# Performance work log

Measured on AMD Instinct MI355X. Metric: run time of the kernel, lower is better.

The kernel has to match this reference:

```python
import jax, jax.numpy as jnp
import numpy as np

B, S, DIM = 2, 2048, 2048
NH, NKV = 16, 4
HD = DIM // NH
BASE, FACTOR = 10000.0, 1.0
WINDOW, STRIDE = 256, 64


def setup_inputs() -> dict:
    key = jax.random.key(0)
    ks = jax.random.split(key, 5)
    x = jax.random.normal(ks[0], (B, S, DIM), jnp.float32)
    Wq = jax.random.normal(ks[1], (DIM, DIM), jnp.float32) * 0.02
    Wkv = jax.random.normal(ks[2], (2 * NKV * HD, DIM), jnp.float32) * 0.02
    Wo = jax.random.normal(ks[3], (DIM, DIM), jnp.float32) * 0.02
    Wr = jax.random.normal(ks[4], (NH, DIM), jnp.float32) * 0.02
    br = jnp.zeros((NH,), jnp.float32)
    return {"x": x, "Wq": Wq, "Wkv": Wkv, "Wo": Wo, "Wr": Wr, "br": br}


def _rope_cos_sin(seqlen, start_pos):
    half = HD // 2
    inv_freq = 1.0 / (BASE ** (jnp.arange(0, half, dtype=jnp.float32) * 2.0 / HD))
    inv_freq = inv_freq / FACTOR  # YaRN position interpolation; FACTOR=1 -> vanilla RoPE
    mscale = float(0.1 * np.log(FACTOR) + 1.0) if FACTOR > 1.0 else 1.0
    t = jnp.arange(start_pos, start_pos + seqlen, dtype=jnp.float32)
    freqs = t[:, None] * inv_freq[None, :]  # [S, HD/2]
    return jnp.cos(freqs) * mscale, jnp.sin(freqs) * mscale


def _apply_rope(x, cos, sin):
    # x: [B, H, S, HD]; rotate-half convention
    x1, x2 = jnp.split(x, 2, axis=-1)
    return jnp.concatenate([x1 * cos - x2 * sin, x2 * cos + x1 * sin], axis=-1)


def reference(x, Wq, Wkv, Wo, Wr, br):
    scale = 1.0 / np.sqrt(HD)
    # projections
    q = (x @ Wq.T).reshape(B, S, NH, HD).transpose(0, 2, 1, 3)        # [B,NH,S,HD]
    kv = (x @ Wkv.T).reshape(B, S, 2, NKV, HD)
    k = kv[:, :, 0].transpose(0, 2, 1, 3)                              # [B,NKV,S,HD]
    v = kv[:, :, 1].transpose(0, 2, 1, 3)
    # RoPE (start_pos = 0)
    cos, sin = _rope_cos_sin(S, 0)
    cos, sin = cos[None, None], sin[None, None]
    q = _apply_rope(q, cos, sin)
    k = _apply_rope(k, cos, sin)
    # GQA expansion (repeat_interleave over head axis)
    rep = NH // NKV
    k = jnp.repeat(k, rep, axis=1)                                     # [B,NH,S,HD]
    v = jnp.repeat(v, rep, axis=1)
    # per-head sigmoid routing gate on q
    head_w = jax.nn.sigmoid(x @ Wr.T + br)                             # [B,S,NH]
    q = q * head_w.transpose(0, 2, 1)[..., None]
    # local windowed causal attention
    qi = jnp.arange(S)[:, None]
    ki = jnp.arange(S)[None, :]
    mask = (ki <= qi) & (ki >= qi - WINDOW)                            # [S,S]
    scores = jnp.einsum('bhqd,bhkd->bhqk', q, k) * scale
    scores = jnp.where(mask, scores, -1e30)
    attn_local = jnp.einsum('bhqk,bhkd->bhqd', jax.nn.softmax(scores, axis=-1), v)
    # strided global attention (non-causal over subsampled keys)
    g_idx = jnp.arange(0, S, STRIDE)
    kg, vg = k[:, :, g_idx], v[:, :, g_idx]                            # [B,NH,S/STRIDE,HD]
    gscores = jnp.einsum('bhqd,bhkd->bhqk', q, kg) * scale
    attn_global = jnp.einsum('bhqk,bhkd->bhqd', jax.nn.softmax(gscores, axis=-1), vg)
    out = 0.7 * attn_local + 0.3 * attn_global
    out = out.transpose(0, 2, 1, 3).reshape(B, S, DIM)
    return out @ Wo.T
```

## Files before the change

kernel.cpp:

```cpp
#include <hip/hip_runtime.h>
#include <stdint.h>

typedef unsigned short u16;
typedef uint32_t u32;
typedef __bf16 bf16x8 __attribute__((ext_vector_type(8)));
typedef u16    u16x8  __attribute__((ext_vector_type(8)));
typedef float  f32x4  __attribute__((ext_vector_type(4)));
typedef u32    u32x4v __attribute__((ext_vector_type(4)));

constexpr int Bc = 2, Sc = 2048, DIMc = 2048, NHc = 16, NKVc = 4, HDc = 128;
constexpr int Mc  = Bc * Sc;
constexpr int QKVN = 3072;
constexpr float SCALE = 0.08838834764831845f;

__device__ __forceinline__ u16 f2bf(float f) {
    uint32_t u = __builtin_bit_cast(uint32_t, f);
    u += 0x7FFFu + ((u >> 16) & 1u);
    return (u16)(u >> 16);
}
__device__ __forceinline__ u32 pk2bf(float a, float b) {
    return (u32)f2bf(a) | ((u32)f2bf(b) << 16);
}

__device__ __forceinline__ void async_cp16(const u16* gsrc, u16* ldst) {
    __builtin_amdgcn_global_load_lds(
        (__attribute__((address_space(1))) void*)(gsrc),
        (__attribute__((address_space(3))) void*)(ldst), 16, 0, 0);
}

constexpr int HWB = Mc;
constexpr int CQ1 = DIMc * DIMc / 4;
constexpr int CQ2 = 1024 * DIMc / 4;
constexpr int CQ3 = DIMc * DIMc / 4;
constexpr int NWQ = (CQ1 + CQ2 + CQ3) / 256;
constexpr int NTB = Sc * 64 / 256;
__global__ __launch_bounds__(256) void cvt_hw(const float* __restrict__ x,
                                              const float* __restrict__ Wq,
                                              const float* __restrict__ Wkv,
                                              const float* __restrict__ Wo,
                                              const float* __restrict__ Wr,
                                              const float* __restrict__ br,
                                              u16* __restrict__ xb,
                                              u16* __restrict__ Wqkvb,
                                              u16* __restrict__ Wob,
                                              float* __restrict__ hw,
                                              float2* __restrict__ csT) {
    __shared__ __align__(16) float xs[2048];
    int bid = blockIdx.x;
    if (bid < HWB) {
        const int m = bid;
        const float4* xg = (const float4*)(x + (size_t)m * 2048);
        float4* xs4 = (float4*)xs;
        for (int i = threadIdx.x; i < 512; i += 256) xs4[i] = xg[i];
        __syncthreads();
        {
            ushort4* dst = (ushort4*)(xb + (size_t)m * 2048);
            for (int i = threadIdx.x; i < 512; i += 256) {
                float4 v = xs4[i];
                ushort4 o;
                o.x = f2bf(v.x); o.y = f2bf(v.y); o.z = f2bf(v.z); o.w = f2bf(v.w);
                dst[i] = o;
            }
        }
        const int wid = threadIdx.x >> 6, lane = threadIdx.x & 63;
#pragma unroll 1
        for (int h = wid; h < NHc; h += 4) {
            const float4* wr4 = (const float4*)(Wr + (size_t)h * 2048);
            float s = 0.f;
#pragma unroll
            for (int j = 0; j < 8; j++) {
                float4 xv = xs4[lane + j * 64];
                float4 wv = wr4[lane + j * 64];
                s += xv.x * wv.x + xv.y * wv.y + xv.z * wv.z + xv.w * wv.w;
            }
#pragma unroll
            for (int off = 32; off; off >>= 1) s += __shfl_xor(s, off, 64);
            if (lane == 0) hw[m * NHc + h] = 1.f / (1.f + __expf(-(s + br[h])));
        }
        return;
    }
    bid -= HWB;
    if (bid < NWQ) {
        int q = bid * 256 + threadIdx.x;
        const float* src; u16* dst; int qi;
        if (q < CQ1)                 { src = Wq;  dst = Wqkvb; qi = q; }
        else if ((q -= CQ1) < CQ2)   { src = Wkv; dst = Wqkvb + (size_t)DIMc * DIMc; qi = q; }
        else                         { q -= CQ2;  src = Wo;  dst = Wob; qi = q; }
        float4 v = ((const float4*)src)[qi];
        ushort4 o;
        o.x = f2bf(v.x); o.y = f2bf(v.y); o.z = f2bf(v.z); o.w = f2bf(v.w);
        ((ushort4*)dst)[qi] = o;
        return;
    }
    bid -= NWQ;
    int idx = bid * 256 + threadIdx.x;
    int s = idx >> 6, d = idx & 63;
    float invf = powf(10000.0f, -(float)d * (1.0f / 64.0f));
    float ang = (float)s * invf;
    float2 cs;
    cs.x = cosf(ang);
    cs.y = sinf(ang);
    csT[idx] = cs;
}

__global__ __launch_bounds__(512, 2) void gemm_qkv(const u16* __restrict__ A,
                                                   const u16* __restrict__ Bw,
                                                   const float* __restrict__ hw,
                                                   const float2* __restrict__ csT,
                                                   u16* __restrict__ Qr,
                                                   u16* __restrict__ Kb,
                                                   u16* __restrict__ Vt,
                                                   u16* __restrict__ Vg) {
    __shared__ __align__(16) u16 SM[4][2][128 * 64];
    float* EpS = (float*)SM;
    const int Kd = DIMc;
    constexpr int NT = 32;
    const int tid  = threadIdx.x;
    const int lane = tid & 63;
    const int wid  = tid >> 6;
    const int m0 = blockIdx.y * 256;
    const int n0 = blockIdx.x * 256;
    const int wr = wid >> 2;
    const int wc = wid & 3;
    const int fr = lane & 15;
    const int fq = lane >> 4;
    const int f7 = fr & 7;

    const int s0 = tid, s1 = tid + 512;
    const int r0 = s0 >> 3, r1 = s1 >> 3;
    const int j0 = (s0 & 7) ^ (r0 & 7), j1 = (s1 & 7) ^ (r1 & 7);
    const u16* gA0 = A  + (size_t)(m0 + r0) * Kd + j0 * 8;
    const u16* gA1 = A  + (size_t)(m0 + r1) * Kd + j1 * 8;
    const u16* gB0 = Bw + (size_t)(n0 + r0) * Kd + j0 * 8;
    const u16* gB1 = Bw + (size_t)(n0 + r1) * Kd + j1 * 8;
    const size_t hK = (size_t)128 * Kd;

    auto stA = [&](int buf, int h, int t) {
        async_cp16(gA0 + h * hK + t * 64, &SM[buf][h][s0 * 8]);
        async_cp16(gA1 + h * hK + t * 64, &SM[buf][h][s1 * 8]);
    };
    auto stB = [&](int buf, int h, int t) {
        async_cp16(gB0 + h * hK + t * 64, &SM[2 + buf][h][s0 * 8]);
        async_cp16(gB1 + h * hK + t * 64, &SM[2 + buf][h][s1 * 8]);
    };

    f32x4 acc[8][4];
#pragma unroll
    for (int i = 0; i < 8; i++)
#pragma unroll
        for (int j = 0; j < 4; j++) {
            f32x4 z = {0.f, 0.f, 0.f, 0.f};
            acc[i][j] = z;
        }

    const int c0 = ((fq) ^ f7) * 8;
    const int c1 = ((4 + fq) ^ f7) * 8;
    bf16x8 afl[4][2], afh[4][2], bfl[2][2], bfh[2][2];

    auto rdA = [&](bf16x8 (&af)[4][2], int tb, int mh) {
        const u16* Ab = SM[tb][wr];
#pragma unroll
        for (int m2 = 0; m2 < 4; m2++) {
            int row = (mh * 4 + m2) * 16 + fr;
            af[m2][0] = __builtin_bit_cast(bf16x8, *(const u16x8*)(Ab + row * 64 + c0));
            af[m2][1] = __builtin_bit_cast(bf16x8, *(const u16x8*)(Ab + row * 64 + c1));
        }
    };
    auto rdB = [&](bf16x8 (&bf)[2][2], int tb, int nh) {
        const u16* Bb = SM[2 + tb][wc >> 1];
#pragma unroll
        for (int n2 = 0; n2 < 2; n2++) {
            int row = (wc & 1) * 64 + (nh * 2 + n2) * 16 + fr;
            bf[n2][0] = __builtin_bit_cast(bf16x8, *(const u16x8*)(Bb + row * 64 + c0));
            bf[n2][1] = __builtin_bit_cast(bf16x8, *(const u16x8*)(Bb + row * 64 + c1));
        }
    };
    auto mma = [&](bf16x8 (&af)[4][2], bf16x8 (&bf)[2][2], int mh, int nh) {
        __builtin_amdgcn_s_setprio(1);
#pragma unroll
        for (int m2 = 0; m2 < 4; m2++)
#pragma unroll
            for (int n2 = 0; n2 < 2; n2++) {
                acc[mh * 4 + m2][nh * 2 + n2] =
                    __builtin_amdgcn_mfma_f32_16x16x32_bf16(af[m2][0], bf[n2][0],
                                                            acc[mh * 4 + m2][nh * 2 + n2], 0, 0, 0);
                acc[mh * 4 + m2][nh * 2 + n2] =
                    __builtin_amdgcn_mfma_f32_16x16x32_bf16(af[m2][1], bf[n2][1],
                                                            acc[mh * 4 + m2][nh * 2 + n2], 0, 0, 0);
            }
        __builtin_amdgcn_s_setprio(0);
    };

#define LGK0 do { asm volatile("s_waitcnt lgkmcnt(0)" ::: "memory"); \
                  __builtin_amdgcn_sched_barrier(0); } while (0)
#define BAR  __builtin_amdgcn_s_barrier()

    stA(0, 0, 0); stA(0, 1, 0); stB(0, 0, 0); stB(0, 1, 0);
    stB(1, 0, 1); stB(1, 1, 1);
    asm volatile("s_waitcnt vmcnt(4)" ::: "memory");
    BAR;

#pragma unroll 1
    for (int i = 0; i < NT / 2; i++) {
        const int t0 = 2 * i, t1 = 2 * i + 1;
        rdA(afl, 0, 0); rdB(bfl, 0, 0);
        stA(1, 0, t1);
        BAR; LGK0; mma(afl, bfl, 0, 0); BAR;
        rdB(bfh, 0, 1);
        stA(1, 1, t1);
        BAR; LGK0; mma(afl, bfh, 0, 1); BAR;
        rdA(afh, 0, 1);
        if (t0 + 2 < NT) stB(0, 0, t0 + 2);
        BAR; LGK0; mma(afh, bfl, 1, 0); BAR;
        if (t0 + 2 < NT) {
            stB(0, 1, t0 + 2);
            asm volatile("s_waitcnt vmcnt(4)" ::: "memory");
        } else {
            asm volatile("s_waitcnt vmcnt(0)" ::: "memory");
        }
        BAR; __builtin_amdgcn_sched_barrier(0); mma(afh, bfh, 1, 1); BAR;
        rdA(afl, 1, 0); rdB(bfl, 1, 0);
        if (t0 + 2 < NT) stA(0, 0, t0 + 2);
        BAR; LGK0; mma(afl, bfl, 0, 0); BAR;
        rdB(bfh, 1, 1);
        if (t0 + 2 < NT) stA(0, 1, t0 + 2);
        BAR; LGK0; mma(afl, bfh, 0, 1); BAR;
        rdA(afh, 1, 1);
        if (t1 + 2 < NT) stB(1, 0, t1 + 2);
        BAR; LGK0; mma(afh, bfl, 1, 0); BAR;
        if (t1 + 2 < NT) {
            stB(1, 1, t1 + 2);
            asm volatile("s_waitcnt vmcnt(4)" ::: "memory");
        } else {
            asm volatile("s_waitcnt vmcnt(0)" ::: "memory");
        }
        BAR; __builtin_amdgcn_sched_barrier(0); mma(afh, bfh, 1, 1); BAR;
    }
#undef LGK0
#undef BAR

    const int tL = n0 >> 7;
    const int bb = m0 >> 11;
    const int sb_t = m0 & 2047;
#pragma unroll
    for (int p = 0; p < 4; p++) {
        __syncthreads();
        if (wr == (p >> 1)) {
#pragma unroll
            for (int m2 = 0; m2 < 4; m2++) {
#pragma unroll
                for (int nj = 0; nj < 4; nj++) {
                    int lr = m2 * 16 + fq * 4;
                    int col = wc * 64 + nj * 16 + fr;
#pragma unroll
                    for (int r = 0; r < 4; r++)
                        EpS[(lr + r) * 261 + col] = acc[(p & 1) * 4 + m2][nj][r];
                }
            }
        }
        __syncthreads();
        const int sbase = sb_t + p * 64;
        if (tL < 20) {
            const int d = tid & 63, rg = tid >> 6;
#pragma unroll 1
            for (int ch = 0; ch < 2; ch++) {
                const int t = tL + ch;
#pragma unroll
                for (int tt = 0; tt < 8; tt++) {
                    int lr = rg + 8 * tt;
                    int s = sbase + lr;
                    float v1 = EpS[lr * 261 + ch * 128 + d];
                    float v2 = EpS[lr * 261 + ch * 128 + 64 + d];
                    float2 cs = csT[(s << 6) + d];
                    float o1 = v1 * cs.x - v2 * cs.y;
                    float o2 = v2 * cs.x + v1 * cs.y;
                    if (t < 16) {
                        float w = hw[(size_t)((bb << 11) + s) * NHc + t] * SCALE;
                        size_t g = ((size_t)(bb * NHc + t) << 11) + s;
                        Qr[g * HDc + d]      = f2bf(o1 * w);
                        Qr[g * HDc + 64 + d] = f2bf(o2 * w);
                    } else {
                        size_t g = ((size_t)(bb * NKVc + (t - 16)) << 11) + s;
                        Kb[g * HDc + d]      = f2bf(o1);
                        Kb[g * HDc + 64 + d] = f2bf(o2);
                    }
                }
            }
        } else {
            const int sl = tid & 63, dg = tid >> 6;
            const int sg = sbase + sl;
#pragma unroll 1
            for (int ch = 0; ch < 2; ch++) {
                const int bhv = bb * NKVc + (tL + ch - 20);
                u16* Vbase = Vt + (size_t)bhv * HDc * Sc;
#pragma unroll
                for (int tt = 0; tt < 16; tt++) {
                    int d = dg + 8 * tt;
                    u16 bv = f2bf(EpS[sl * 261 + ch * 128 + d]);
                    Vbase[(size_t)d * Sc + sg] = bv;
                    if ((sg & 63) == 0)
                        Vg[(size_t)bhv * 4096 + d * 32 + (sg >> 6)] = bv;
                }
            }
        }
    }
}

__global__ __launch_bounds__(512, 2) void gemm_bt3(const u16* __restrict__ A,
                                                   const u16* __restrict__ Bw,
                                                   float* __restrict__ C,
                                                   int Mdim, int Ndim, int Kdim) {
    __shared__ __align__(16) u16 As[2][256 * 64];
    __shared__ __align__(16) u16 Bs[2][128 * 64];
    const int tid  = threadIdx.x;
    const int lane = tid & 63;
    const int wid  = tid >> 6;
    const int m0 = blockIdx.y * 256;
    const int n0 = blockIdx.x * 128;
    const int wm = (wid >> 1) * 64;
    const int wn = (wid & 1) * 64;
    const int fr = lane & 15;
    const int fq = lane >> 4;
    const int f7 = fr & 7;

    const u16* gA[4]; const u16* gB[2];
    int sOffA[4], sOffB[2];
#pragma unroll
    for (int q = 0; q < 4; q++) {
        int s = tid + q * 512;
        int row = s >> 3;
        int j = (s & 7) ^ (row & 7);
        gA[q] = A + (size_t)(m0 + row) * Kdim + j * 8;
        sOffA[q] = s * 8;
    }
#pragma unroll
    for (int q = 0; q < 2; q++) {
        int s = tid + q * 512;
        int row = s >> 3;
        int j = (s & 7) ^ (row & 7);
        gB[q] = Bw + (size_t)(n0 + row) * Kdim + j * 8;
        sOffB[q] = s * 8;
    }

    f32x4 acc[4][4];
#pragma unroll
    for (int i = 0; i < 4; i++)
#pragma unroll
        for (int j = 0; j < 4; j++) {
            f32x4 z = {0.f, 0.f, 0.f, 0.f};
            acc[i][j] = z;
        }

    const int NT = Kdim >> 6;
    const int c0 = ((fq) ^ f7) * 8;
    const int c1 = ((4 + fq) ^ f7) * 8;

#pragma unroll
    for (int q = 0; q < 4; q++) async_cp16(gA[q], &As[0][sOffA[q]]);
#pragma unroll
    for (int q = 0; q < 2; q++) async_cp16(gB[q], &Bs[0][sOffB[q]]);
#pragma unroll
    for (int q = 0; q < 4; q++) async_cp16(gA[q] + 64, &As[1][sOffA[q]]);
#pragma unroll
    for (int q = 0; q < 2; q++) async_cp16(gB[q] + 64, &Bs[1][sOffB[q]]);

    for (int t = 0; t < NT; t++) {
        const u16* At = As[t & 1];
        const u16* Bt = Bs[t & 1];

        if (t + 1 < NT) {
            asm volatile("s_waitcnt vmcnt(6)" ::: "memory");
        } else {
            asm volatile("s_waitcnt vmcnt(0)" ::: "memory");
        }
        __builtin_amdgcn_s_barrier();

        bf16x8 af0[4], bf0[4];
#pragma unroll
        for (int i = 0; i < 4; i++)
            af0[i] = __builtin_bit_cast(bf16x8, *(const u16x8*)(At + (wm + i * 16 + fr) * 64 + c0));
#pragma unroll
        for (int j = 0; j < 4; j++)
            bf0[j] = __builtin_bit_cast(bf16x8, *(const u16x8*)(Bt + (wn + j * 16 + fr) * 64 + c0));
        asm volatile("s_waitcnt lgkmcnt(0)" ::: "memory");
        __builtin_amdgcn_sched_barrier(0);
        __builtin_amdgcn_s_setprio(1);
#pragma unroll
        for (int i = 0; i < 2; i++)
#pragma unroll
            for (int j = 0; j < 4; j++)
                acc[i][j] = __builtin_amdgcn_mfma_f32_16x16x32_bf16(af0[i], bf0[j], acc[i][j], 0, 0, 0);
        __builtin_amdgcn_s_setprio(0);

        bf16x8 af1[4], bf1[4];
#pragma unroll
        for (int i = 0; i < 4; i++)
            af1[i] = __builtin_bit_cast(bf16x8, *(const u16x8*)(At + (wm + i * 16 + fr) * 64 + c1));
#pragma unroll
        for (int j = 0; j < 4; j++)
            bf1[j] = __builtin_bit_cast(bf16x8, *(const u16x8*)(Bt + (wn + j * 16 + fr) * 64 + c1));
        __builtin_amdgcn_s_setprio(1);
#pragma unroll
        for (int i = 2; i < 4; i++)
#pragma unroll
            for (int j = 0; j < 4; j++)
                acc[i][j] = __builtin_amdgcn_mfma_f32_16x16x32_bf16(af0[i], bf0[j], acc[i][j], 0, 0, 0);
        __builtin_amdgcn_s_setprio(0);
        asm volatile("s_waitcnt lgkmcnt(0)" ::: "memory");
        __builtin_amdgcn_sched_barrier(0);
        __builtin_amdgcn_s_barrier();

        if (t + 2 < NT) {
#pragma unroll
            for (int q = 0; q < 4; q++)
                async_cp16(gA[q] + (size_t)(t + 2) * 64, &As[t & 1][sOffA[q]]);
        }
        __builtin_amdgcn_s_setprio(1);
#pragma unroll
        for (int i = 0; i < 2; i++)
#pragma unroll
            for (int j = 0; j < 4; j++)
                acc[i][j] = __builtin_amdgcn_mfma_f32_16x16x32_bf16(af1[i], bf1[j], acc[i][j], 0, 0, 0);
        __builtin_amdgcn_s_setprio(0);

        if (t + 2 < NT) {
#pragma unroll
            for (int q = 0; q < 2; q++)
                async_cp16(gB[q] + (size_t)(t + 2) * 64, &Bs[t & 1][sOffB[q]]);
        }
        __builtin_amdgcn_s_setprio(1);
#pragma unroll
        for (int i = 2; i < 4; i++)
#pragma unroll
            for (int j = 0; j < 4; j++)
                acc[i][j] = __builtin_amdgcn_mfma_f32_16x16x32_bf16(af1[i], bf1[j], acc[i][j], 0, 0, 0);
        __builtin_amdgcn_s_setprio(0);
    }

#pragma unroll
    for (int i = 0; i < 4; i++)
#pragma unroll
        for (int j = 0; j < 4; j++) {
            int row = m0 + wm + i * 16 + fq * 4;
            int col = n0 + wn + j * 16 + fr;
#pragma unroll
            for (int r = 0; r < 4; r++)
                C[(size_t)(row + r) * Ndim + col] = acc[i][j][r];
        }
}

__device__ __forceinline__ float colreduce_max(f32x4 a, f32x4 b) {
    float m = fmaxf(fmaxf(fmaxf(a[0], a[1]), fmaxf(a[2], a[3])),
                    fmaxf(fmaxf(b[0], b[1]), fmaxf(b[2], b[3])));
    m = fmaxf(m, __shfl_xor(m, 16, 64));
    m = fmaxf(m, __shfl_xor(m, 32, 64));
    return m;
}

__device__ __forceinline__ bf16x8 build_pfrag(u32 pk0, u32 pk1, u32 pk2, u32 pk3, int lane) {
    const int c = lane & 15, Q = lane >> 4;
    const int sl0 = ((Q & 1) * 2) * 16 + c;
    const int sl1 = sl0 + 16;
    u32 a0 = (u32)__shfl((int)pk0, sl0, 64), b0 = (u32)__shfl((int)pk2, sl0, 64);
    u32 a1 = (u32)__shfl((int)pk1, sl0, 64), b1 = (u32)__shfl((int)pk3, sl0, 64);
    u32 a2 = (u32)__shfl((int)pk0, sl1, 64), b2 = (u32)__shfl((int)pk2, sl1, 64);
    u32 a3 = (u32)__shfl((int)pk1, sl1, 64), b3 = (u32)__shfl((int)pk3, sl1, 64);
    const bool hi = Q >= 2;
    u32x4v r = { hi ? b0 : a0, hi ? b1 : a1, hi ? b2 : a2, hi ? b3 : a3 };
    return __builtin_bit_cast(bf16x8, r);
}

__global__ __launch_bounds__(256) void attn3(const u16* __restrict__ Qr,
                                             const u16* __restrict__ Kb,
                                             const u16* __restrict__ Vt,
                                             const u16* __restrict__ Vg,
                                             u16* __restrict__ attnb) {
    __shared__ __align__(16) u16 Ksh[2 * 4096];
    __shared__ __align__(16) u16 Vsh[2 * 4096];
    const int tid  = threadIdx.x;
    const int lane = tid & 63, wid = tid >> 6;
    const int bid  = blockIdx.x;
    const int q64  = (31 - (bid >> 5)) << 6;
    const int bh   = bid & 31;
    const int h    = bh & 15;
    const int b    = bh >> 4;
    const int qw   = q64 + wid * 16;
    const int c = lane & 15, Q = lane >> 4;
    const int kvh = h >> 2;

    const u16* Qp = Qr + ((size_t)((b * NHc + h) * Sc + qw)) * HDc;
    const u16* Kh = Kb + (size_t)(b * NKVc + kvh) * Sc * HDc;
    const u16* Vh = Vt + (size_t)(b * NKVc + kvh) * HDc * Sc;
    const u16* Vgh = Vg + (size_t)(b * NKVc + kvh) * HDc * 32;

    const int kp0 = (q64 >= 256) ? (q64 - 256) : 0;
    const int nstages = (q64 + 64 - kp0) >> 5;

    auto stageLoad = [&](int bufi, int kp) {
        u16* Kd = Ksh + bufi * 4096;
        u16* Vd = Vsh + bufi * 4096;
#pragma unroll
        for (int qq = 0; qq < 2; qq++) {
            int s = tid + qq * 256;
            int kr = s >> 4;
            int jk = (s & 15) ^ (kr & 15);
            async_cp16(Kh + (size_t)(kp + kr) * HDc + jk * 8, Kd + s * 8);
            int dv = s >> 2;
            int jv = (s & 3) ^ ((dv >> 2) & 3);
            async_cp16(Vh + (size_t)dv * Sc + kp + jv * 8, Vd + s * 8);
        }
    };

    bf16x8 qf[4];
#pragma unroll
    for (int ch = 0; ch < 4; ch++)
        qf[ch] = __builtin_bit_cast(bf16x8, *(const u16x8*)(Qp + c * HDc + ch * 32 + Q * 8));

    stageLoad(0, kp0);

    f32x4 sg0 = {0.f,0.f,0.f,0.f}, sg1 = {0.f,0.f,0.f,0.f};
#pragma unroll
    for (int ch = 0; ch < 4; ch++) {
        bf16x8 k0 = __builtin_bit_cast(bf16x8, *(const u16x8*)(Kh + ((size_t)c << 6) * HDc + ch * 32 + Q * 8));
        bf16x8 k1 = __builtin_bit_cast(bf16x8, *(const u16x8*)(Kh + ((size_t)(c + 16) << 6) * HDc + ch * 32 + Q * 8));
        sg0 = __builtin_amdgcn_mfma_f32_16x16x32_bf16(k0, qf[ch], sg0, 0, 0, 0);
        sg1 = __builtin_amdgcn_mfma_f32_16x16x32_bf16(k1, qf[ch], sg1, 0, 0, 0);
    }
    float mg = colreduce_max(sg0, sg1);
    f32x4 pg0, pg1;
    float gsum = 0.f;
#pragma unroll
    for (int r = 0; r < 4; r++) {
        pg0[r] = __expf(sg0[r] - mg);
        pg1[r] = __expf(sg1[r] - mg);
        gsum += pg0[r] + pg1[r];
    }
    gsum += __shfl_xor(gsum, 16, 64);
    gsum += __shfl_xor(gsum, 32, 64);
    const float lG = gsum;
    bf16x8 pgf = build_pfrag(pk2bf(pg0[0], pg0[1]), pk2bf(pg0[2], pg0[3]),
                             pk2bf(pg1[0], pg1[1]), pk2bf(pg1[2], pg1[3]), lane);
    f32x4 OG[8];
#pragma unroll
    for (int dt = 0; dt < 8; dt++) {
        bf16x8 vf = __builtin_bit_cast(bf16x8, *(const u16x8*)(Vgh + (dt * 16 + c) * 32 + Q * 8));
        f32x4 z = {0.f, 0.f, 0.f, 0.f};
        OG[dt] = __builtin_amdgcn_mfma_f32_16x16x32_bf16(vf, pgf, z, 0, 0, 0);
    }

    f32x4 OL[8];
#pragma unroll
    for (int dt = 0; dt < 8; dt++) { f32x4 z = {0.f,0.f,0.f,0.f}; OL[dt] = z; }
    float mL = -1e30f, lL = 0.f;

    for (int ip = 0; ip < nstages; ip++) {
        const int kp = kp0 + ip * 32;
        __syncthreads();
        if (ip + 1 < nstages) stageLoad((ip + 1) & 1, kp + 32);
        const u16* Kd = Ksh + (ip & 1) * 4096;
        const u16* Vd = Vsh + (ip & 1) * 4096;

        if (kp > qw + 15 || kp + 31 < qw - 256) continue;

        f32x4 s0 = {0.f,0.f,0.f,0.f}, s1 = {0.f,0.f,0.f,0.f};
#pragma unroll
        for (int ch = 0; ch < 4; ch++) {
            int jj = ch * 4 + Q;
            bf16x8 k0 = __builtin_bit_cast(bf16x8, *(const u16x8*)(Kd + (c * 16 + (jj ^ c)) * 8));
            bf16x8 k1 = __builtin_bit_cast(bf16x8, *(const u16x8*)(Kd + ((16 + c) * 16 + (jj ^ c)) * 8));
            s0 = __builtin_amdgcn_mfma_f32_16x16x32_bf16(k0, qf[ch], s0, 0, 0, 0);
            s1 = __builtin_amdgcn_mfma_f32_16x16x32_bf16(k1, qf[ch], s1, 0, 0, 0);
        }
        if ((kp + 31 > qw) || (kp < qw - 241)) {
            const int q = qw + c;
#pragma unroll
            for (int r = 0; r < 4; r++) {
                int kk0 = kp + Q * 4 + r;
                int kk1 = kk0 + 16;
                if (kk0 > q || kk0 + 256 < q) s0[r] = -1e30f;
                if (kk1 > q || kk1 + 256 < q) s1[r] = -1e30f;
            }
        }
        float mx = colreduce_max(s0, s1);
        float mnew = fmaxf(mL, mx);
        float alpha = __expf(mL - mnew);
        f32x4 p0, p1;
        float sum = 0.f;
#pragma unroll
        for (int r = 0; r < 4; r++) {
            p0[r] = __expf(s0[r] - mnew);
            p1[r] = __expf(s1[r] - mnew);
            sum += p0[r] + p1[r];
        }
        sum += __shfl_xor(sum, 16, 64);
        sum += __shfl_xor(sum, 32, 64);
        lL = lL * alpha + sum;
        mL = mnew;
        bf16x8 pf = build_pfrag(pk2bf(p0[0], p0[1]), pk2bf(p0[2], p0[3]),
                                pk2bf(p1[0], p1[1]), pk2bf(p1[2], p1[3]), lane);
#pragma unroll
        for (int dt = 0; dt < 8; dt++) {
            int d = dt * 16 + c;
            bf16x8 vf = __builtin_bit_cast(bf16x8, *(const u16x8*)(Vd + (d * 4 + (Q ^ (c >> 2))) * 8));
            OL[dt] = OL[dt] * alpha;
            OL[dt] = __builtin_amdgcn_mfma_f32_16x16x32_bf16(vf, pf, OL[dt], 0, 0, 0);
        }
    }

    const float rL = 0.7f / lL, rG = 0.3f / lG;
    u16* orow = attnb + ((size_t)(b * Sc + qw + c)) * DIMc + h * HDc;
#pragma unroll
    for (int dt = 0; dt < 8; dt++) {
        ushort4 ov;
        ov.x = f2bf(OL[dt][0] * rL + OG[dt][0] * rG);
        ov.y = f2bf(OL[dt][1] * rL + OG[dt][1] * rG);
        ov.z = f2bf(OL[dt][2] * rL + OG[dt][2] * rG);
        ov.w = f2bf(OL[dt][3] * rL + OG[dt][3] * rG);
        *(ushort4*)(orow + dt * 16 + Q * 4) = ov;
    }
}

extern "C" void kernel_launch(void* const* d_in, const int* in_sizes, int n_in,
                              void* d_out, int out_size, void* d_ws, size_t ws_size,
                              hipStream_t stream) {
    const float* x   = (const float*)d_in[0];
    const float* Wq  = (const float*)d_in[1];
    const float* Wkv = (const float*)d_in[2];
    const float* Wo  = (const float*)d_in[3];
    const float* Wr  = (const float*)d_in[4];
    const float* br  = (const float*)d_in[5];
    float* out = (float*)d_out;

    char* p = (char*)d_ws;
    u16* xb    = (u16*)p;   p += (size_t)Mc * DIMc * 2;
    u16* Wqkvb = (u16*)p;   p += (size_t)QKVN * DIMc * 2;
    u16* Wob   = (u16*)p;   p += (size_t)DIMc * DIMc * 2;
    float* hw  = (float*)p; p += (size_t)Mc * NHc * 4;
    float2* csT = (float2*)p; p += (size_t)Sc * 64 * 8;
    u16* Qrb   = (u16*)p;   p += (size_t)Mc * DIMc * 2;
    u16* Kb16  = (u16*)p;   p += (size_t)Bc * NKVc * Sc * HDc * 2;
    u16* Vt16  = (u16*)p;   p += (size_t)Bc * NKVc * HDc * Sc * 2;
    u16* Vg16  = (u16*)p;   p += (size_t)Bc * NKVc * HDc * 32 * 2;
    u16* attnb = (u16*)p;   p += (size_t)Mc * DIMc * 2;

    cvt_hw<<<HWB + NWQ + NTB, 256, 0, stream>>>(x, Wq, Wkv, Wo, Wr, br, xb, Wqkvb, Wob, hw, csT);

    dim3 gqkv(QKVN / 256, Mc / 256);
    gemm_qkv<<<gqkv, 512, 0, stream>>>(xb, Wqkvb, hw, csT, Qrb, Kb16, Vt16, Vg16);

    attn3<<<Bc * NHc * (Sc / 64), 256, 0, stream>>>(Qrb, Kb16, Vt16, Vg16, attnb);

    dim3 go(DIMc / 128, Mc / 256);
    gemm_bt3<<<go, 512, 0, stream>>>(attnb, Wob, out, Mc, DIMc, DIMc);
}
```

Baseline: 286.8 us.

## Restructure GEMM main loop into per-tile double-buffered pipeline with fewer barriers

Replaces the two-tile unrolled loop, which put a barrier pair around each of its eight MFMA quarter-blocks, with a single-tile loop. Each iteration issues all four LDS fragment reads up front, waits on partial lgkmcnt counts so MFMAs start as fragments arrive, and refills the freed buffer half with global loads for tile t+2. The intent is to cut barrier and LDS-wait stalls and overlap LDS reads with MFMA. In exchange it holds more fragments in flight, relies on exact vmcnt/lgkmcnt accounting, and prefetches both A and B for tile 1 in the prologue.

```diff
diff --git a/kernel.cpp b/kernel.cpp
--- a/kernel.cpp
+++ b/kernel.cpp
@@ -191,52 +191,43 @@
         __builtin_amdgcn_s_setprio(0);
     };
 
-#define LGK0 do { asm volatile("s_waitcnt lgkmcnt(0)" ::: "memory"); \
-                  __builtin_amdgcn_sched_barrier(0); } while (0)
+#define SB   __builtin_amdgcn_sched_barrier(0)
 #define BAR  __builtin_amdgcn_s_barrier()
 
     stA(0, 0, 0); stA(0, 1, 0); stB(0, 0, 0); stB(0, 1, 0);
-    stB(1, 0, 1); stB(1, 1, 1);
-    asm volatile("s_waitcnt vmcnt(4)" ::: "memory");
-    BAR;
+    stA(1, 0, 1); stA(1, 1, 1); stB(1, 0, 1); stB(1, 1, 1);
 
 #pragma unroll 1
-    for (int i = 0; i < NT / 2; i++) {
-        const int t0 = 2 * i, t1 = 2 * i + 1;
-        rdA(afl, 0, 0); rdB(bfl, 0, 0);
-        stA(1, 0, t1);
-        BAR; LGK0; mma(afl, bfl, 0, 0); BAR;
-        rdB(bfh, 0, 1);
-        stA(1, 1, t1);
-        BAR; LGK0; mma(afl, bfh, 0, 1); BAR;
-        rdA(afh, 0, 1);
-        if (t0 + 2 < NT) stB(0, 0, t0 + 2);
-        BAR; LGK0; mma(afh, bfl, 1, 0); BAR;
-        if (t0 + 2 < NT) {
-            stB(0, 1, t0 + 2);
-            asm volatile("s_waitcnt vmcnt(4)" ::: "memory");
+    for (int t = 0; t < NT; t++) {
+        const int b = t & 1;
+        if (t + 1 < NT) {
+            asm volatile("s_waitcnt vmcnt(8)" ::: "memory");
         } else {
             asm volatile("s_waitcnt vmcnt(0)" ::: "memory");
         }
-        BAR; __builtin_amdgcn_sched_barrier(0); mma(afh, bfh, 1, 1); BAR;
-        rdA(afl, 1, 0); rdB(bfl, 1, 0);
-        if (t0 + 2 < NT) stA(0, 0, t0 + 2);
-        BAR; LGK0; mma(afl, bfl, 0, 0); BAR;
-        rdB(bfh, 1, 1);
-        if (t0 + 2 < NT) stA(0, 1, t0 + 2);
-        BAR; LGK0; mma(afl, bfh, 0, 1); BAR;
-        rdA(afh, 1, 1);
-        if (t1 + 2 < NT) stB(1, 0, t1 + 2);
-        BAR; LGK0; mma(afh, bfl, 1, 0); BAR;
-        if (t1 + 2 < NT) {
-            stB(1, 1, t1 + 2);
-            asm volatile("s_waitcnt vmcnt(4)" ::: "memory");
-        } else {
-            asm volatile("s_waitcnt vmcnt(0)" ::: "memory");
-        }
-        BAR; __builtin_amdgcn_sched_barrier(0); mma(afh, bfh, 1, 1); BAR;
-    }
-#undef LGK0
+        BAR; SB;
+
+        rdA(afl, b, 0);
+        rdB(bfl, b, 0);
+        rdB(bfh, b, 1);
+        rdA(afh, b, 1);
+
+        asm volatile("s_waitcnt lgkmcnt(12)" ::: "memory"); SB;
+        mma(afl, bfl, 0, 0);
+        asm volatile("s_waitcnt lgkmcnt(8)" ::: "memory"); SB;
+        mma(afl, bfh, 0, 1);
+
+        BAR; SB;
+        if (t + 2 < NT) { stB(b, 0, t + 2); stB(b, 1, t + 2); }
+
+        asm volatile("s_waitcnt lgkmcnt(0)" ::: "memory"); SB;
+        mma(afh, bfl, 1, 0);
+
+        BAR; SB;
+        if (t + 2 < NT) { stA(b, 0, t + 2); stA(b, 1, t + 2); }
+        mma(afh, bfh, 1, 1);
+    }
+#undef SB
 #undef BAR
 
     const int tL = n0 >> 7;
```

New measurement: 287.1 us. No clear change (+0.1%).
